# Kernel optimization log

Hardware: AMD Instinct MI355X
Metric: run time of the kernel (lower is better)

The kernel has to match this reference:

```python
import jax, jax.numpy as jnp
import numpy as np

B, T, H, K, V, O = 4, 2048, 512, 128, 128, 512


def setup_inputs() -> dict:
    key = jax.random.key(0)
    k0, k1, k2 = jax.random.split(key, 3)
    hidden_state = jax.random.normal(k0, (B, T, H), dtype=jnp.float32)
    cell_state = jnp.zeros((B, K, V), dtype=jnp.float32)
    # fused projection: hidden -> [query K, key K, gate K, value V]
    lim_p = np.sqrt(6.0 / (H + 3 * K + V)).astype(np.float32)  # xavier uniform
    proj_w = jax.random.uniform(k1, (3 * K + V, H), jnp.float32, -lim_p, lim_p)
    proj_b = jnp.zeros((3 * K + V,), jnp.float32)
    lim_o = np.sqrt(6.0 / (2 * V + O)).astype(np.float32)
    out_w = jax.random.uniform(k2, (O, 2 * V), jnp.float32, -lim_o, lim_o)
    out_b = jnp.zeros((O,), jnp.float32)
    return {"hidden_state": hidden_state, "cell_state": cell_state,
            "proj_w": proj_w, "proj_b": proj_b, "out_w": out_w, "out_b": out_b}


def reference(hidden_state, cell_state, proj_w, proj_b, out_w, out_b):
    Bq, Tq, _ = hidden_state.shape
    qkgv = hidden_state @ proj_w.T + proj_b          # (B,T,3K+V)
    query = qkgv[..., :K]
    kgate = jax.nn.sigmoid(qkgv[..., K:2 * K])       # key (sigmoid)
    gate = jax.nn.sigmoid(qkgv[..., 2 * K:3 * K])
    value = jnp.tanh(qkgv[..., 3 * K:])              # (B,T,V)

    def step(C, xs):
        q_t, k_t, g_t, v_t = xs                      # (B,K),(B,K),(B,K),(B,V)
        C = C * g_t[..., None] + k_t[..., None] * v_t[..., None, :]  # (B,K,V)
        o_t = jnp.einsum('bkv,bk->bv', C, q_t)       # C^T q
        return C, o_t

    xs = (query.swapaxes(0, 1), kgate.swapaxes(0, 1),
          gate.swapaxes(0, 1), value.swapaxes(0, 1))
    C_final, ov = jax.lax.scan(step, cell_state, xs)
    ov = ov.swapaxes(0, 1)                           # (B,T,V) output_val per step

    # causal Luong dot attention over the growing bank of past output_vals
    scores = jnp.einsum('btv,bsv->bts', ov, ov)      # (B,T,T)
    causal = jnp.tril(jnp.ones((Tq, Tq), dtype=bool))
    scores = jnp.where(causal, scores, -jnp.inf)
    attn = jax.nn.softmax(scores, axis=-1)
    context = jnp.einsum('bts,bsv->btv', attn, ov)   # (B,T,V)

    outputs = jnp.concatenate([ov, context], axis=-1) @ out_w.T + out_b  # (B,T,O)
    return outputs, C_final
```

## Files before the change

kernel.cpp:

```cpp
#include <hip/hip_runtime.h>
#include <hip/hip_bf16.h>


typedef __attribute__((ext_vector_type(8))) short bf16x8;
typedef __attribute__((ext_vector_type(4))) float f32x4;
typedef __attribute__((ext_vector_type(4))) short short4v;

#define MFMA(a,b,c) __builtin_amdgcn_mfma_f32_16x16x32_bf16(a,b,c,0,0,0)

__device__ __forceinline__ short f2b(float x){
  union { float f; unsigned u; } v; v.f = x;
  unsigned r = v.u + 0x7fffu + ((v.u >> 16) & 1u);
  return (short)(r >> 16);
}
__device__ __forceinline__ float b2f(short h){
  union { unsigned u; float f; } v;
  v.u = ((unsigned)(unsigned short)h) << 16;
  return v.f;
}
__device__ __forceinline__ void split2(float x, short& h, short& l){
  h = f2b(x);
  l = f2b(x - b2f(h));
}

__global__ void k_split(const float* __restrict__ in, short* __restrict__ hi,
                        short* __restrict__ lo, int n){
  int i = (blockIdx.x * blockDim.x + threadIdx.x) * 4;
  if (i < n){
    float4 v = *(const float4*)(in + i);
    short4v h, l;
    short th, tl;
    split2(v.x, th, tl); h.x = th; l.x = tl;
    split2(v.y, th, tl); h.y = th; l.y = tl;
    split2(v.z, th, tl); h.z = th; l.z = tl;
    split2(v.w, th, tl); h.w = th; l.w = tl;
    *(short4v*)(hi + i) = h;
    *(short4v*)(lo + i) = l;
  }
}

__global__ void k_cvt(const float* __restrict__ in, short* __restrict__ out, int n){
  int i = (blockIdx.x * blockDim.x + threadIdx.x) * 4;
  if (i < n){
    float4 v = *(const float4*)(in + i);
    short4v o; o.x = f2b(v.x); o.y = f2b(v.y); o.z = f2b(v.z); o.w = f2b(v.w);
    *(short4v*)(out + i) = o;
  }
}

__global__ __launch_bounds__(256) void k_gemm1(
    const short* __restrict__ Ah, const short* __restrict__ Al,
    const short* __restrict__ Bh, const short* __restrict__ Bl,
    const float* __restrict__ bias,
    float* __restrict__ q_o, float* __restrict__ kg_o,
    float* __restrict__ lg_o, float* __restrict__ vv_o)
{
  const int Kd = 512;
  __shared__ __align__(16) short Ash[128][40], Asl[128][40];
  __shared__ __align__(16) short Bsh[64][40],  Bsl[64][40];
  const int m0 = blockIdx.x * 128, n0 = blockIdx.y * 64;
  const int tid = threadIdx.x, lane = tid & 63, w = tid >> 6;
  const int wr = w >> 1, wc = w & 1;
  const int coll = lane & 15, rq = lane >> 4;
  f32x4 acc[4][2];
#pragma unroll
  for (int i = 0; i < 4; i++)
#pragma unroll
    for (int j = 0; j < 2; j++) acc[i][j] = (f32x4){0.f,0.f,0.f,0.f};

  const int ar = tid >> 1, ac = (tid & 1) * 16;
  const int br = tid >> 2, bc = (tid & 3) * 8;

  for (int k0 = 0; k0 < Kd; k0 += 32){
    __syncthreads();
    { size_t g = (size_t)(m0 + ar) * Kd + k0 + ac;
      *(bf16x8*)&Ash[ar][ac]     = *(const bf16x8*)(Ah + g);
      *(bf16x8*)&Ash[ar][ac + 8] = *(const bf16x8*)(Ah + g + 8);
      *(bf16x8*)&Asl[ar][ac]     = *(const bf16x8*)(Al + g);
      *(bf16x8*)&Asl[ar][ac + 8] = *(const bf16x8*)(Al + g + 8); }
    { size_t g = (size_t)(n0 + br) * Kd + k0 + bc;
      *(bf16x8*)&Bsh[br][bc] = *(const bf16x8*)(Bh + g);
      *(bf16x8*)&Bsl[br][bc] = *(const bf16x8*)(Bl + g); }
    __syncthreads();
    bf16x8 ah[4], al[4], bh[2], bl[2];
#pragma unroll
    for (int mi = 0; mi < 4; mi++){
      ah[mi] = *(const bf16x8*)&Ash[wr*64 + mi*16 + coll][rq*8];
      al[mi] = *(const bf16x8*)&Asl[wr*64 + mi*16 + coll][rq*8];
    }
#pragma unroll
    for (int ni = 0; ni < 2; ni++){
      bh[ni] = *(const bf16x8*)&Bsh[wc*32 + ni*16 + coll][rq*8];
      bl[ni] = *(const bf16x8*)&Bsl[wc*32 + ni*16 + coll][rq*8];
    }
#pragma unroll
    for (int mi = 0; mi < 4; mi++)
#pragma unroll
      for (int ni = 0; ni < 2; ni++){
        acc[mi][ni] = MFMA(ah[mi], bh[ni], acc[mi][ni]);
        acc[mi][ni] = MFMA(ah[mi], bl[ni], acc[mi][ni]);
        acc[mi][ni] = MFMA(al[mi], bh[ni], acc[mi][ni]);
      }
  }
#pragma unroll
  for (int mi = 0; mi < 4; mi++)
#pragma unroll
  for (int ni = 0; ni < 2; ni++){
    int gn = n0 + wc*32 + ni*16 + coll;
    float bsv = bias[gn];
    int sec = gn >> 7, jj = gn & 127;
#pragma unroll
    for (int r = 0; r < 4; r++){
      int gm = m0 + wr*64 + mi*16 + rq*4 + r;
      float v = acc[mi][ni][r] + bsv;
      size_t idx = (size_t)gm * 128 + jj;
      if (sec == 0)      q_o[idx] = v;
      else if (sec == 1) kg_o[idx] = 1.f / (1.f + __expf(-v));
      else if (sec == 2) lg_o[idx] = (v > 0.f) ? -log1pf(__expf(-v)) : (v - log1pf(__expf(v)));
      else               vv_o[idx] = tanhf(v);
    }
  }
}

__global__ __launch_bounds__(128) void k_prep(
  const float* __restrict__ q_f, const float* __restrict__ kg_f,
  const float* __restrict__ lg_f, const float* __restrict__ vv_f,
  short* __restrict__ qth, short* __restrict__ qtl,
  short* __restrict__ kth, short* __restrict__ ktl,
  short* __restrict__ khTh, short* __restrict__ khTl,
  short* __restrict__ vvTh, short* __restrict__ vvTl,
  float* __restrict__ Dend)
{
  const int bc = blockIdx.x;
  const int kx = threadIdx.x;
  const size_t base = ((size_t)(bc >> 6) * 2048 + (size_t)(bc & 63) * 32) * 128 + kx;
  double L[32];
  double Lr = 0.0;
#pragma unroll
  for (int s = 0; s < 32; s++){
    size_t idx = base + (size_t)s * 128;
    Lr += (double)lg_f[idx];
    L[s] = Lr;
    float lam  = __expf((float)Lr);
    float ilam = __expf((float)(-Lr));
    short h, l;
    split2(q_f[idx] * lam, h, l);  qth[idx] = h; qtl[idx] = l;
    split2(kg_f[idx] * ilam, h, l); kth[idx] = h; ktl[idx] = l;
  }
  const double Lend = Lr;
  Dend[(size_t)bc * 128 + kx] = (float)exp(Lend);
  __align__(16) short bufh[32], bufl[32];
#pragma unroll
  for (int s = 0; s < 32; s++){
    size_t idx = base + (size_t)s * 128;
    short h, l;
    split2(kg_f[idx] * __expf((float)(Lend - L[s])), h, l);
    bufh[s] = h; bufl[s] = l;
  }
  { short* dh = khTh + ((size_t)bc * 128 + kx) * 32;
    short* dl = khTl + ((size_t)bc * 128 + kx) * 32;
#pragma unroll
    for (int i = 0; i < 32; i += 8){
      *(bf16x8*)(dh + i) = *(const bf16x8*)(bufh + i);
      *(bf16x8*)(dl + i) = *(const bf16x8*)(bufl + i);
    } }
#pragma unroll
  for (int s = 0; s < 32; s++){
    short h, l;
    split2(vv_f[base + (size_t)s * 128], h, l);
    bufh[s] = h; bufl[s] = l;
  }
  { short* dh = vvTh + ((size_t)bc * 128 + kx) * 32;
    short* dl = vvTl + ((size_t)bc * 128 + kx) * 32;
#pragma unroll
    for (int i = 0; i < 32; i += 8){
      *(bf16x8*)(dh + i) = *(const bf16x8*)(bufh + i);
      *(bf16x8*)(dl + i) = *(const bf16x8*)(bufl + i);
    } }
}

__global__ __launch_bounds__(64) void k_scan(
  const short* __restrict__ khTh, const short* __restrict__ khTl,
  const short* __restrict__ vvTh, const short* __restrict__ vvTl,
  const float* __restrict__ Dend, const float* __restrict__ cell0,
  short* __restrict__ sth, short* __restrict__ stl, float* __restrict__ Cfin)
{
  const int blk = blockIdx.x;
  const int b = blk >> 6, tile = blk & 63;
  const int kt = tile >> 3, vt = tile & 7;
  const int lane = threadIdx.x & 63;
  const int coll = lane & 15, rq = lane >> 4;
  const int kcol = kt*16 + coll;
  const int vrow0 = vt*16 + rq*4;
  const size_t cb0 = (size_t)b * 64;

  f32x4 acc;
#pragma unroll
  for (int r = 0; r < 4; r++)
    acc[r] = cell0[((size_t)b*128 + kcol)*128 + vrow0 + r];

  size_t gv = (cb0*128 + vt*16 + coll)*32 + rq*8;
  size_t gk = (cb0*128 + kt*16 + coll)*32 + rq*8;
  bf16x8 avh = *(const bf16x8*)(vvTh + gv);
  bf16x8 avl = *(const bf16x8*)(vvTl + gv);
  bf16x8 bkh = *(const bf16x8*)(khTh + gk);
  bf16x8 bkl = *(const bf16x8*)(khTl + gk);
  float d = Dend[cb0*128 + kcol];

  for (int ck = 0; ck < 64; ck++){
    const size_t cb = cb0 + ck;
    const size_t cbn = cb0 + (ck < 63 ? ck + 1 : ck);
    size_t ngv = (cbn*128 + vt*16 + coll)*32 + rq*8;
    size_t ngk = (cbn*128 + kt*16 + coll)*32 + rq*8;
    bf16x8 navh = *(const bf16x8*)(vvTh + ngv);
    bf16x8 navl = *(const bf16x8*)(vvTl + ngv);
    bf16x8 nbkh = *(const bf16x8*)(khTh + ngk);
    bf16x8 nbkl = *(const bf16x8*)(khTl + ngk);
    float nd = Dend[cbn*128 + kcol];
    {
      size_t sb = (cb*128 + vrow0)*128 + kcol;
#pragma unroll
      for (int r = 0; r < 4; r++){
        short h, l; split2(acc[r], h, l);
        sth[sb + (size_t)r*128] = h;
        stl[sb + (size_t)r*128] = l;
      }
    }
#pragma unroll
    for (int r = 0; r < 4; r++) acc[r] *= d;
    acc = MFMA(avh, bkh, acc);
    acc = MFMA(avh, bkl, acc);
    acc = MFMA(avl, bkh, acc);
    avh = navh; avl = navl; bkh = nbkh; bkl = nbkl; d = nd;
  }
  *(f32x4*)(Cfin + ((size_t)b*128 + kcol)*128 + vrow0) = acc;
}

__global__ __launch_bounds__(256) void k_chunkout(
  const short* __restrict__ qth, const short* __restrict__ qtl,
  const short* __restrict__ kth, const short* __restrict__ ktl,
  const short* __restrict__ vvTh, const short* __restrict__ vvTl,
  const short* __restrict__ sth, const short* __restrict__ stl,
  short* __restrict__ ovT, short* __restrict__ ovc,
  short* __restrict__ ovqh, short* __restrict__ ovql)
{
  __shared__ __align__(16) short ATh[32][40], ATl[32][40];
  const int bc = blockIdx.x;
  const int b = bc >> 6, ck = bc & 63;
  const int tid = threadIdx.x, lane = tid & 63, w = tid >> 6;
  const int coll = lane & 15, rq = lane >> 4;
  const size_t tbase = (size_t)b * 2048 + (size_t)ck * 32;
  {
    const int si = w >> 1, ti = w & 1;
    f32x4 aA = (f32x4){0.f,0.f,0.f,0.f};
#pragma unroll
    for (int kit = 0; kit < 4; kit++){
      size_t ga = (tbase + si*16 + coll) * 128 + kit*32 + rq*8;
      size_t gb = (tbase + ti*16 + coll) * 128 + kit*32 + rq*8;
      bf16x8 a3h = *(const bf16x8*)(kth + ga), a3l = *(const bf16x8*)(ktl + ga);
      bf16x8 b3h = *(const bf16x8*)(qth + gb), b3l = *(const bf16x8*)(qtl + gb);
      aA = MFMA(a3h, b3h, aA);
      aA = MFMA(a3h, b3l, aA);
      aA = MFMA(a3l, b3h, aA);
    }
#pragma unroll
    for (int r = 0; r < 4; r++){
      int s = si*16 + rq*4 + r, t = ti*16 + coll;
      float val = (s <= t) ? aA[r] : 0.f;
      short h, l; split2(val, h, l);
      ATh[t][s] = h; ATl[t][s] = l;
    }
  }
  __syncthreads();
  const int vb = w * 32;
  f32x4 o[2][2];
#pragma unroll
  for (int vi = 0; vi < 2; vi++)
#pragma unroll
    for (int ti = 0; ti < 2; ti++) o[vi][ti] = (f32x4){0.f,0.f,0.f,0.f};
#pragma unroll
  for (int kit = 0; kit < 4; kit++){
    bf16x8 aCh[2], aCl[2], bqh[2], bql[2];
#pragma unroll
    for (int vi = 0; vi < 2; vi++){
      size_t g = ((size_t)bc * 128 + vb + vi*16 + coll) * 128 + kit*32 + rq*8;
      aCh[vi] = *(const bf16x8*)(sth + g);
      aCl[vi] = *(const bf16x8*)(stl + g);
    }
#pragma unroll
    for (int ti = 0; ti < 2; ti++){
      size_t g = (tbase + ti*16 + coll) * 128 + kit*32 + rq*8;
      bqh[ti] = *(const bf16x8*)(qth + g);
      bql[ti] = *(const bf16x8*)(qtl + g);
    }
#pragma unroll
    for (int vi = 0; vi < 2; vi++)
#pragma unroll
      for (int ti = 0; ti < 2; ti++){
        o[vi][ti] = MFMA(aCh[vi], bqh[ti], o[vi][ti]);
        o[vi][ti] = MFMA(aCh[vi], bql[ti], o[vi][ti]);
        o[vi][ti] = MFMA(aCl[vi], bqh[ti], o[vi][ti]);
      }
  }
  {
    bf16x8 a2h[2], a2l[2], b2h[2], b2l[2];
#pragma unroll
    for (int vi = 0; vi < 2; vi++){
      size_t g = ((size_t)bc * 128 + vb + vi*16 + coll) * 32 + rq*8;
      a2h[vi] = *(const bf16x8*)(vvTh + g);
      a2l[vi] = *(const bf16x8*)(vvTl + g);
    }
#pragma unroll
    for (int ti = 0; ti < 2; ti++){
      b2h[ti] = *(const bf16x8*)&ATh[ti*16 + coll][rq*8];
      b2l[ti] = *(const bf16x8*)&ATl[ti*16 + coll][rq*8];
    }
#pragma unroll
    for (int vi = 0; vi < 2; vi++)
#pragma unroll
      for (int ti = 0; ti < 2; ti++){
        o[vi][ti] = MFMA(a2h[vi], b2h[ti], o[vi][ti]);
        o[vi][ti] = MFMA(a2h[vi], b2l[ti], o[vi][ti]);
        o[vi][ti] = MFMA(a2l[vi], b2h[ti], o[vi][ti]);
      }
  }
#pragma unroll
  for (int vi = 0; vi < 2; vi++)
#pragma unroll
  for (int ti = 0; ti < 2; ti++)
#pragma unroll
  for (int r = 0; r < 4; r++){
    int v = vb + vi*16 + rq*4 + r;
    int tl = ti*16 + coll;
    float val = o[vi][ti][r];
    short h, l; split2(val, h, l);
    ovT[((size_t)b * 128 + v) * 2048 + (size_t)ck * 32 + tl] = h;
    ovc[(tbase + tl) * 256 + v] = h;
    ovqh[(tbase + tl) * 128 + v] = h;
    ovql[(tbase + tl) * 128 + v] = l;
  }
}

__global__ __launch_bounds__(256) void k_attn(
  const short* __restrict__ ovqh, const short* __restrict__ ovql,
  const short* __restrict__ ovT,
  float* __restrict__ m_part, float* __restrict__ l_part,
  short* __restrict__ oa_part)
{
  const int qi = blockIdx.x, b = blockIdx.y, p = blockIdx.z;
  const int qbase = qi * 64;
  const int ps = p * 256;
  const size_t obase = (size_t)b * 2048;
  const int tid = threadIdx.x;
  if (ps > qbase + 63){
    if (tid < 64) l_part[((obase + qbase + tid) << 3) + p] = 0.f;
    return;
  }
  __shared__ __align__(16) short P[4][16][40];
  const int lane = tid & 63, w = tid >> 6;
  const int coll = lane & 15, rq = lane >> 4;
  const int tw = qbase + w * 16;
  bf16x8 qfh[4], qfl[4];
#pragma unroll
  for (int kit = 0; kit < 4; kit++){
    size_t g = (obase + tw + coll) * 128 + kit*32 + rq*8;
    qfh[kit] = *(const bf16x8*)(ovqh + g);
    qfl[kit] = *(const bf16x8*)(ovql + g);
  }
  float m[4], l[4];
  f32x4 oa[8];
#pragma unroll
  for (int r = 0; r < 4; r++){ m[r] = -1e30f; l[r] = 0.f; }
#pragma unroll
  for (int df = 0; df < 8; df++) oa[df] = (f32x4){0.f,0.f,0.f,0.f};
  const int send = min(tw + 15, ps + 255);
  for (int s0 = ps; s0 <= send; s0 += 32){
    f32x4 sc[2];
#pragma unroll
    for (int sf = 0; sf < 2; sf++){
      bf16x8 kh[4], kl[4];
#pragma unroll
      for (int kit = 0; kit < 4; kit++){
        size_t g = (obase + s0 + sf*16 + coll) * 128 + kit*32 + rq*8;
        kh[kit] = *(const bf16x8*)(ovqh + g);
        kl[kit] = *(const bf16x8*)(ovql + g);
      }
      f32x4 c0 = (f32x4){0.f,0.f,0.f,0.f};
      f32x4 c1 = (f32x4){0.f,0.f,0.f,0.f};
      f32x4 c2 = (f32x4){0.f,0.f,0.f,0.f};
#pragma unroll
      for (int kit = 0; kit < 4; kit++){
        c0 = MFMA(qfh[kit], kh[kit], c0);
        c1 = MFMA(qfh[kit], kl[kit], c1);
        c2 = MFMA(qfl[kit], kh[kit], c2);
      }
      sc[sf] = c0 + c1 + c2;
    }
    bf16x8 vf[8];
#pragma unroll
    for (int df = 0; df < 8; df++)
      vf[df] = *(const bf16x8*)(ovT + ((size_t)b*128 + df*16 + coll)*2048 + s0 + rq*8);
#pragma unroll
    for (int r = 0; r < 4; r++){
      int trow = tw + rq*4 + r;
      float s0v = (s0 + coll      <= trow) ? sc[0][r] : -1e30f;
      float s1v = (s0 + 16 + coll <= trow) ? sc[1][r] : -1e30f;
      float mx = fmaxf(s0v, s1v);
#pragma unroll
      for (int d = 1; d < 16; d <<= 1) mx = fmaxf(mx, __shfl_xor(mx, d));
      float mn = fmaxf(m[r], mx);
      float scale = __expf(m[r] - mn);
      float p0 = __expf(s0v - mn);
      float p1 = __expf(s1v - mn);
      float rs = p0 + p1;
#pragma unroll
      for (int d = 1; d < 16; d <<= 1) rs += __shfl_xor(rs, d);
      l[r] = l[r] * scale + rs;
      m[r] = mn;
#pragma unroll
      for (int df = 0; df < 8; df++) oa[df][r] *= scale;
      P[w][rq*4 + r][coll]      = f2b(p0);
      P[w][rq*4 + r][16 + coll] = f2b(p1);
    }
    bf16x8 pf = *(const bf16x8*)&P[w][coll][rq*8];
#pragma unroll
    for (int df = 0; df < 8; df++)
      oa[df] = MFMA(pf, vf[df], oa[df]);
  }
#pragma unroll
  for (int r = 0; r < 4; r++){
    int t = tw + rq*4 + r;
    size_t idx8 = ((obase + t) << 3) + p;
    if (coll == 0){ m_part[idx8] = m[r]; l_part[idx8] = l[r]; }
#pragma unroll
    for (int df = 0; df < 8; df++)
      oa_part[idx8*128 + df*16 + coll] = f2b(oa[df][r]);
  }
}

__global__ __launch_bounds__(256) void k_comb(
  const float* __restrict__ m_part, const float* __restrict__ l_part,
  const short* __restrict__ oa_part, short* __restrict__ ovc)
{
  const int blk = blockIdx.x;
  const int b = blk >> 5, qi = blk & 31;
  const int row = threadIdx.x >> 2, cg = threadIdx.x & 3;
  const int t = qi*64 + row;
  const size_t base8 = ((size_t)b*2048 + t) * 8;
  float mv[8], lv[8];
#pragma unroll
  for (int p = 0; p < 8; p++){ mv[p] = m_part[base8+p]; lv[p] = l_part[base8+p]; }
  float M = -3e38f;
#pragma unroll
  for (int p = 0; p < 8; p++) if (lv[p] > 0.f) M = fmaxf(M, mv[p]);
  float L = 0.f, wgt[8];
#pragma unroll
  for (int p = 0; p < 8; p++){
    wgt[p] = (lv[p] > 0.f) ? __expf(mv[p] - M) : 0.f;
    L += lv[p] * wgt[p];
  }
  const float inv = 1.f / L;
  const int v0 = cg * 32;
  float acc[32];
#pragma unroll
  for (int j = 0; j < 32; j++) acc[j] = 0.f;
#pragma unroll
  for (int p = 0; p < 8; p++){
    if (lv[p] > 0.f){
      const short* src = oa_part + (base8 + p)*128 + v0;
#pragma unroll
      for (int jo = 0; jo < 32; jo += 8){
        bf16x8 x = *(const bf16x8*)(src + jo);
#pragma unroll
        for (int j = 0; j < 8; j++) acc[jo+j] += b2f(x[j]) * wgt[p];
      }
    }
  }
  short* dst = ovc + ((size_t)b*2048 + t)*256 + 128 + v0;
#pragma unroll
  for (int jo = 0; jo < 32; jo += 8){
    bf16x8 o;
#pragma unroll
    for (int j = 0; j < 8; j++) o[j] = f2b(acc[jo+j] * inv);
    *(bf16x8*)(dst + jo) = o;
  }
}

__global__ __launch_bounds__(256) void k_gemm0(
  const short* __restrict__ A, const short* __restrict__ Bw,
  const float* __restrict__ bias, float* __restrict__ out)
{
  const int Kd = 256, N = 512;
  __shared__ __align__(16) short As[128][40];
  __shared__ __align__(16) short Bs[64][40];
  const int m0 = blockIdx.x * 128, n0 = blockIdx.y * 64;
  const int tid = threadIdx.x, lane = tid & 63, w = tid >> 6;
  const int wr = w >> 1, wc = w & 1;
  const int coll = lane & 15, rq = lane >> 4;
  f32x4 acc[4][2];
#pragma unroll
  for (int i = 0; i < 4; i++)
#pragma unroll
    for (int j = 0; j < 2; j++) acc[i][j] = (f32x4){0.f,0.f,0.f,0.f};
  const int ar = tid >> 1, ac = (tid & 1) * 16;
  const int br = tid >> 2, bc = (tid & 3) * 8;
  for (int k0 = 0; k0 < Kd; k0 += 32){
    __syncthreads();
    { const short* g = A + (size_t)(m0 + ar) * Kd + k0 + ac;
      *(bf16x8*)&As[ar][ac]     = *(const bf16x8*)g;
      *(bf16x8*)&As[ar][ac + 8] = *(const bf16x8*)(g + 8); }
    { const short* g = Bw + (size_t)(n0 + br) * Kd + k0 + bc;
      *(bf16x8*)&Bs[br][bc] = *(const bf16x8*)g; }
    __syncthreads();
    bf16x8 a[4], b[2];
#pragma unroll
    for (int mi = 0; mi < 4; mi++) a[mi] = *(const bf16x8*)&As[wr*64 + mi*16 + coll][rq*8];
#pragma unroll
    for (int ni = 0; ni < 2; ni++) b[ni] = *(const bf16x8*)&Bs[wc*32 + ni*16 + coll][rq*8];
#pragma unroll
    for (int mi = 0; mi < 4; mi++)
#pragma unroll
      for (int ni = 0; ni < 2; ni++) acc[mi][ni] = MFMA(a[mi], b[ni], acc[mi][ni]);
  }
#pragma unroll
  for (int mi = 0; mi < 4; mi++)
#pragma unroll
  for (int ni = 0; ni < 2; ni++){
    int gn = n0 + wc*32 + ni*16 + coll;
    float bsv = bias[gn];
#pragma unroll
    for (int r = 0; r < 4; r++){
      int gm = m0 + wr*64 + mi*16 + rq*4 + r;
      out[(size_t)gm * N + gn] = acc[mi][ni][r] + bsv;
    }
  }
}

extern "C" void kernel_launch(void* const* d_in, const int* in_sizes, int n_in,
                              void* d_out, int out_size, void* d_ws, size_t ws_size,
                              hipStream_t stream){
  const float* hidden = (const float*)d_in[0];
  const float* cell0  = (const float*)d_in[1];
  const float* projw  = (const float*)d_in[2];
  const float* projb  = (const float*)d_in[3];
  const float* outw   = (const float*)d_in[4];
  const float* outb   = (const float*)d_in[5];
  float* out = (float*)d_out;

  char* ws = (char*)d_ws;
  size_t off = 0;
  auto alloc = [&](size_t bytes) -> void* {
    void* p = ws + off;
    off += (bytes + 255) & ~(size_t)255;
    return p;
  };
  short* Xh   = (short*)alloc(8192ULL * 512 * 2);
  short* Xl   = (short*)alloc(8192ULL * 512 * 2);
  short* ovqh = Xh;
  short* ovql = Xh + 1048576;
  short* ovT  = Xh + 2097152;
  short* ovc  = Xh + 3145728;
  float* q_f  = (float*)alloc(8192ULL * 128 * 4);
  float* kg_f = (float*)alloc(8192ULL * 128 * 4);
  float* lg_f = (float*)alloc(8192ULL * 128 * 4);
  float* vv_f = (float*)alloc(8192ULL * 128 * 4);
  short* sth  = (short*)q_f;
  short* stl  = sth + 4194304;
  short* oa_part = (short*)q_f;
  short* Wh   = (short*)alloc(512ULL * 512 * 2);
  short* Wl   = (short*)alloc(512ULL * 512 * 2);
  short* OWbf = (short*)alloc(512ULL * 256 * 2);
  short* qth  = (short*)alloc(8192ULL * 128 * 2);
  short* qtl  = (short*)alloc(8192ULL * 128 * 2);
  short* kth  = (short*)alloc(8192ULL * 128 * 2);
  short* ktl  = (short*)alloc(8192ULL * 128 * 2);
  short* khTh = (short*)alloc(256ULL * 128 * 32 * 2);
  short* khTl = (short*)alloc(256ULL * 128 * 32 * 2);
  short* vvTh = (short*)alloc(256ULL * 128 * 32 * 2);
  short* vvTl = (short*)alloc(256ULL * 128 * 32 * 2);
  float* Dend = (float*)alloc(256ULL * 128 * 4);
  float* m_part = (float*)alloc(4ULL * 2048 * 8 * 4);
  float* l_part = (float*)alloc(4ULL * 2048 * 8 * 4);

  k_split<<<4096, 256, 0, stream>>>(hidden, Xh, Xl, 8192 * 512);
  k_split<<<256,  256, 0, stream>>>(projw,  Wh, Wl, 512 * 512);
  k_cvt<<<128, 256, 0, stream>>>(outw, OWbf, 512 * 256);

  k_gemm1<<<dim3(64, 8), 256, 0, stream>>>(Xh, Xl, Wh, Wl, projb, q_f, kg_f, lg_f, vv_f);
  k_prep<<<256, 128, 0, stream>>>(q_f, kg_f, lg_f, vv_f,
                                  qth, qtl, kth, ktl, khTh, khTl, vvTh, vvTl, Dend);
  k_scan<<<256, 64, 0, stream>>>(khTh, khTl, vvTh, vvTl, Dend, cell0,
                                 sth, stl, out + 8192ULL * 512);
  k_chunkout<<<256, 256, 0, stream>>>(qth, qtl, kth, ktl, vvTh, vvTl, sth, stl,
                                      ovT, ovc, ovqh, ovql);
  k_attn<<<dim3(32, 4, 8), 256, 0, stream>>>(ovqh, ovql, ovT, m_part, l_part, oa_part);
  k_comb<<<128, 256, 0, stream>>>(m_part, l_part, oa_part, ovc);
  k_gemm0<<<dim3(64, 8), 256, 0, stream>>>(ovc, OWbf, outb, out);
}
```

Baseline: 293.8 us.

## Use direct global-to-LDS loads with XOR-swizzled tiles in projection and output GEMMs

Both bf16 GEMM kernels now stage tiles with global_load_lds 16-byte direct copies into unpadded 64-wide LDS tiles, using an XOR swizzle to avoid bank conflicts instead of row padding. The K-step grows from 32 to 64, which halves the barrier count. The split-precision GEMM is restructured into three sequential passes over K (hi*hi, hi*lo, lo*hi) instead of three MFMAs per loaded tile. This removes the register round-trip for global loads but adds more total A/B traffic in gemm1, since each operand is reloaded per pass, and there is still no double buffering.

New measurement: 293.8 us. Within noise of the previous version (-0.0%).

```diff
diff --git a/kernel.cpp b/kernel.cpp
--- a/kernel.cpp
+++ b/kernel.cpp
@@ -21,6 +21,11 @@
 __device__ __forceinline__ void split2(float x, short& h, short& l){
   h = f2b(x);
   l = f2b(x - b2f(h));
+}
+__device__ __forceinline__ void gload16(const void* g, void* l){
+  __builtin_amdgcn_global_load_lds(
+    (__attribute__((address_space(1))) unsigned int*)(void*)(g),
+    (__attribute__((address_space(3))) unsigned int*)(l), 16, 0, 0);
 }
 
 __global__ void k_split(const float* __restrict__ in, short* __restrict__ hi,
@@ -55,10 +60,10 @@
     float* __restrict__ q_o, float* __restrict__ kg_o,
     float* __restrict__ lg_o, float* __restrict__ vv_o)
 {
-  const int Kd = 512;
-  __shared__ __align__(16) short Ash[128][40], Asl[128][40];
-  __shared__ __align__(16) short Bsh[64][40],  Bsl[64][40];
-  const int m0 = blockIdx.x * 128, n0 = blockIdx.y * 64;
+  __shared__ __align__(16) short At[128*64];
+  __shared__ __align__(16) short Bt[64*64];
+  const int m0 = blockIdx.x * 128;
+  const int ny = blockIdx.y;
   const int tid = threadIdx.x, lane = tid & 63, w = tid >> 6;
   const int wr = w >> 1, wc = w & 1;
   const int coll = lane & 15, rq = lane >> 4;
@@ -68,47 +73,56 @@
 #pragma unroll
     for (int j = 0; j < 2; j++) acc[i][j] = (f32x4){0.f,0.f,0.f,0.f};
 
-  const int ar = tid >> 1, ac = (tid & 1) * 16;
-  const int br = tid >> 2, bc = (tid & 3) * 8;
-
-  for (int k0 = 0; k0 < Kd; k0 += 32){
+  for (int step = 0; step < 24; ++step){
+    const int seg = step >> 3;
+    const int k0 = (step & 7) * 64;
+    const short* Asrc = (seg < 2) ? Ah : Al;
+    const short* Bsrc = (seg == 1) ? Bl : Bh;
     __syncthreads();
-    { size_t g = (size_t)(m0 + ar) * Kd + k0 + ac;
-      *(bf16x8*)&Ash[ar][ac]     = *(const bf16x8*)(Ah + g);
-      *(bf16x8*)&Ash[ar][ac + 8] = *(const bf16x8*)(Ah + g + 8);
-      *(bf16x8*)&Asl[ar][ac]     = *(const bf16x8*)(Al + g);
-      *(bf16x8*)&Asl[ar][ac + 8] = *(const bf16x8*)(Al + g + 8); }
-    { size_t g = (size_t)(n0 + br) * Kd + k0 + bc;
-      *(bf16x8*)&Bsh[br][bc] = *(const bf16x8*)(Bh + g);
-      *(bf16x8*)&Bsl[br][bc] = *(const bf16x8*)(Bl + g); }
+#pragma unroll
+    for (int t = 0; t < 4; ++t){
+      int ci = t*256 + tid;
+      int row = ci >> 3;
+      int cs = (ci & 7) ^ (row & 7);
+      gload16(Asrc + (size_t)(m0 + row)*512 + k0 + cs*8, At + ci*8);
+    }
+#pragma unroll
+    for (int t = 0; t < 2; ++t){
+      int ci = t*256 + tid;
+      int row = ci >> 3;
+      int cs = (ci & 7) ^ (row & 7);
+      gload16(Bsrc + (size_t)(ny*64 + row)*512 + k0 + cs*8, Bt + ci*8);
+    }
     __syncthreads();
-    bf16x8 ah[4], al[4], bh[2], bl[2];
-#pragma unroll
-    for (int mi = 0; mi < 4; mi++){
-      ah[mi] = *(const bf16x8*)&Ash[wr*64 + mi*16 + coll][rq*8];
-      al[mi] = *(const bf16x8*)&Asl[wr*64 + mi*16 + coll][rq*8];
-    }
-#pragma unroll
-    for (int ni = 0; ni < 2; ni++){
-      bh[ni] = *(const bf16x8*)&Bsh[wc*32 + ni*16 + coll][rq*8];
-      bl[ni] = *(const bf16x8*)&Bsl[wc*32 + ni*16 + coll][rq*8];
-    }
-#pragma unroll
-    for (int mi = 0; mi < 4; mi++)
+#pragma unroll
+    for (int kk = 0; kk < 2; ++kk){
+      bf16x8 a[4], b[2];
+#pragma unroll
+      for (int mi = 0; mi < 4; mi++){
+        int ar = wr*64 + mi*16 + coll;
+        a[mi] = *(const bf16x8*)&At[ar*64 + (((kk*4+rq) ^ (ar & 7))*8)];
+      }
 #pragma unroll
       for (int ni = 0; ni < 2; ni++){
-        acc[mi][ni] = MFMA(ah[mi], bh[ni], acc[mi][ni]);
-        acc[mi][ni] = MFMA(ah[mi], bl[ni], acc[mi][ni]);
-        acc[mi][ni] = MFMA(al[mi], bh[ni], acc[mi][ni]);
-      }
-  }
+        int br = wc*32 + ni*16 + coll;
+        b[ni] = *(const bf16x8*)&Bt[br*64 + (((kk*4+rq) ^ (br & 7))*8)];
+      }
+#pragma unroll
+      for (int mi = 0; mi < 4; mi++)
+#pragma unroll
+        for (int ni = 0; ni < 2; ni++)
+          acc[mi][ni] = MFMA(a[mi], b[ni], acc[mi][ni]);
+    }
+  }
+  const int sec = ny >> 1;
+  const int jb  = (ny & 1) * 64;
 #pragma unroll
   for (int mi = 0; mi < 4; mi++)
 #pragma unroll
   for (int ni = 0; ni < 2; ni++){
-    int gn = n0 + wc*32 + ni*16 + coll;
-    float bsv = bias[gn];
-    int sec = gn >> 7, jj = gn & 127;
+    int gl = wc*32 + ni*16 + coll;
+    float bsv = bias[ny*64 + gl];
+    int jj = jb + gl;
 #pragma unroll
     for (int r = 0; r < 4; r++){
       int gm = m0 + wr*64 + mi*16 + rq*4 + r;
@@ -490,10 +504,10 @@
   const short* __restrict__ A, const short* __restrict__ Bw,
   const float* __restrict__ bias, float* __restrict__ out)
 {
-  const int Kd = 256, N = 512;
-  __shared__ __align__(16) short As[128][40];
-  __shared__ __align__(16) short Bs[64][40];
-  const int m0 = blockIdx.x * 128, n0 = blockIdx.y * 64;
+  __shared__ __align__(16) short At[128*64];
+  __shared__ __align__(16) short Bt[64*64];
+  const int m0 = blockIdx.x * 128;
+  const int ny = blockIdx.y;
   const int tid = threadIdx.x, lane = tid & 63, w = tid >> 6;
   const int wr = w >> 1, wc = w & 1;
   const int coll = lane & 15, rq = lane >> 4;
@@ -502,36 +516,55 @@
   for (int i = 0; i < 4; i++)
 #pragma unroll
     for (int j = 0; j < 2; j++) acc[i][j] = (f32x4){0.f,0.f,0.f,0.f};
-  const int ar = tid >> 1, ac = (tid & 1) * 16;
-  const int br = tid >> 2, bc = (tid & 3) * 8;
-  for (int k0 = 0; k0 < Kd; k0 += 32){
+
+  for (int step = 0; step < 4; ++step){
+    const int k0 = step * 64;
     __syncthreads();
-    { const short* g = A + (size_t)(m0 + ar) * Kd + k0 + ac;
-      *(bf16x8*)&As[ar][ac]     = *(const bf16x8*)g;
-      *(bf16x8*)&As[ar][ac + 8] = *(const bf16x8*)(g + 8); }
-    { const short* g = Bw + (size_t)(n0 + br) * Kd + k0 + bc;
-      *(bf16x8*)&Bs[br][bc] = *(const bf16x8*)g; }
+#pragma unroll
+    for (int t = 0; t < 4; ++t){
+      int ci = t*256 + tid;
+      int row = ci >> 3;
+      int cs = (ci & 7) ^ (row & 7);
+      gload16(A + (size_t)(m0 + row)*256 + k0 + cs*8, At + ci*8);
+    }
+#pragma unroll
+    for (int t = 0; t < 2; ++t){
+      int ci = t*256 + tid;
+      int row = ci >> 3;
+      int cs = (ci & 7) ^ (row & 7);
+      gload16(Bw + (size_t)(ny*64 + row)*256 + k0 + cs*8, Bt + ci*8);
+    }
     __syncthreads();
-    bf16x8 a[4], b[2];
-#pragma unroll
-    for (int mi = 0; mi < 4; mi++) a[mi] = *(const bf16x8*)&As[wr*64 + mi*16 + coll][rq*8];
-#pragma unroll
-    for (int ni = 0; ni < 2; ni++) b[ni] = *(const bf16x8*)&Bs[wc*32 + ni*16 + coll][rq*8];
-#pragma unroll
-    for (int mi = 0; mi < 4; mi++)
-#pragma unroll
-      for (int ni = 0; ni < 2; ni++) acc[mi][ni] = MFMA(a[mi], b[ni], acc[mi][ni]);
+#pragma unroll
+    for (int kk = 0; kk < 2; ++kk){
+      bf16x8 a[4], b[2];
+#pragma unroll
+      for (int mi = 0; mi < 4; mi++){
+        int ar = wr*64 + mi*16 + coll;
+        a[mi] = *(const bf16x8*)&At[ar*64 + (((kk*4+rq) ^ (ar & 7))*8)];
+      }
+#pragma unroll
+      for (int ni = 0; ni < 2; ni++){
+        int br = wc*32 + ni*16 + coll;
+        b[ni] = *(const bf16x8*)&Bt[br*64 + (((kk*4+rq) ^ (br & 7))*8)];
+      }
+#pragma unroll
+      for (int mi = 0; mi < 4; mi++)
+#pragma unroll
+        for (int ni = 0; ni < 2; ni++)
+          acc[mi][ni] = MFMA(a[mi], b[ni], acc[mi][ni]);
+    }
   }
 #pragma unroll
   for (int mi = 0; mi < 4; mi++)
 #pragma unroll
   for (int ni = 0; ni < 2; ni++){
-    int gn = n0 + wc*32 + ni*16 + coll;
+    int gn = ny*64 + wc*32 + ni*16 + coll;
     float bsv = bias[gn];
 #pragma unroll
     for (int r = 0; r < 4; r++){
       int gm = m0 + wr*64 + mi*16 + rq*4 + r;
-      out[(size_t)gm * N + gn] = acc[mi][ni][r] + bsv;
+      out[(size_t)gm * 512 + gn] = acc[mi][ni][r] + bsv;
     }
   }
 }
```

## Drop LDS staging in projection GEMMs, load MFMA fragments straight from global

Applied to the files above, without the earlier changes.

Both GEMM kernels (the input projection with split-bf16 and the output projection) stop staging tiles in shared memory with barriers. Instead each wave loads its MFMA operand fragments directly from global memory and computes a 64x64 tile, with a block covering 64 rows by 256 columns. This removes the __syncthreads and LDS round trips. In exchange it depends on L1/L2 to absorb repeated A-row loads across the four waves, and it issues less coalesced 16-byte-per-lane global reads.

After: 395.7 us. 34.7% more time.

```diff
diff --git a/kernel.cpp b/kernel.cpp
--- a/kernel.cpp
+++ b/kernel.cpp
@@ -55,63 +55,51 @@
     float* __restrict__ q_o, float* __restrict__ kg_o,
     float* __restrict__ lg_o, float* __restrict__ vv_o)
 {
-  const int Kd = 512;
-  __shared__ __align__(16) short Ash[128][40], Asl[128][40];
-  __shared__ __align__(16) short Bsh[64][40],  Bsl[64][40];
-  const int m0 = blockIdx.x * 128, n0 = blockIdx.y * 64;
   const int tid = threadIdx.x, lane = tid & 63, w = tid >> 6;
-  const int wr = w >> 1, wc = w & 1;
   const int coll = lane & 15, rq = lane >> 4;
-  f32x4 acc[4][2];
+  const int m0 = blockIdx.x * 64;
+  const int n0 = blockIdx.y * 256 + w * 64;
+  f32x4 acc[4][4];
 #pragma unroll
   for (int i = 0; i < 4; i++)
 #pragma unroll
-    for (int j = 0; j < 2; j++) acc[i][j] = (f32x4){0.f,0.f,0.f,0.f};
-
-  const int ar = tid >> 1, ac = (tid & 1) * 16;
-  const int br = tid >> 2, bc = (tid & 3) * 8;
-
-  for (int k0 = 0; k0 < Kd; k0 += 32){
-    __syncthreads();
-    { size_t g = (size_t)(m0 + ar) * Kd + k0 + ac;
-      *(bf16x8*)&Ash[ar][ac]     = *(const bf16x8*)(Ah + g);
-      *(bf16x8*)&Ash[ar][ac + 8] = *(const bf16x8*)(Ah + g + 8);
-      *(bf16x8*)&Asl[ar][ac]     = *(const bf16x8*)(Al + g);
-      *(bf16x8*)&Asl[ar][ac + 8] = *(const bf16x8*)(Al + g + 8); }
-    { size_t g = (size_t)(n0 + br) * Kd + k0 + bc;
-      *(bf16x8*)&Bsh[br][bc] = *(const bf16x8*)(Bh + g);
-      *(bf16x8*)&Bsl[br][bc] = *(const bf16x8*)(Bl + g); }
-    __syncthreads();
-    bf16x8 ah[4], al[4], bh[2], bl[2];
+    for (int j = 0; j < 4; j++) acc[i][j] = (f32x4){0.f,0.f,0.f,0.f};
+
+#pragma unroll 2
+  for (int k0 = 0; k0 < 512; k0 += 32){
+    bf16x8 ah[4], al[4], bh[4], bl[4];
 #pragma unroll
     for (int mi = 0; mi < 4; mi++){
-      ah[mi] = *(const bf16x8*)&Ash[wr*64 + mi*16 + coll][rq*8];
-      al[mi] = *(const bf16x8*)&Asl[wr*64 + mi*16 + coll][rq*8];
-    }
-#pragma unroll
-    for (int ni = 0; ni < 2; ni++){
-      bh[ni] = *(const bf16x8*)&Bsh[wc*32 + ni*16 + coll][rq*8];
-      bl[ni] = *(const bf16x8*)&Bsl[wc*32 + ni*16 + coll][rq*8];
+      size_t g = (size_t)(m0 + mi*16 + coll)*512 + k0 + rq*8;
+      ah[mi] = *(const bf16x8*)(Ah + g);
+      al[mi] = *(const bf16x8*)(Al + g);
+    }
+#pragma unroll
+    for (int ni = 0; ni < 4; ni++){
+      size_t g = (size_t)(n0 + ni*16 + coll)*512 + k0 + rq*8;
+      bh[ni] = *(const bf16x8*)(Bh + g);
+      bl[ni] = *(const bf16x8*)(Bl + g);
     }
 #pragma unroll
     for (int mi = 0; mi < 4; mi++)
 #pragma unroll
-      for (int ni = 0; ni < 2; ni++){
+      for (int ni = 0; ni < 4; ni++){
         acc[mi][ni] = MFMA(ah[mi], bh[ni], acc[mi][ni]);
         acc[mi][ni] = MFMA(ah[mi], bl[ni], acc[mi][ni]);
         acc[mi][ni] = MFMA(al[mi], bh[ni], acc[mi][ni]);
       }
   }
+  const int sec = n0 >> 7;
 #pragma unroll
   for (int mi = 0; mi < 4; mi++)
 #pragma unroll
-  for (int ni = 0; ni < 2; ni++){
-    int gn = n0 + wc*32 + ni*16 + coll;
-    float bsv = bias[gn];
-    int sec = gn >> 7, jj = gn & 127;
+  for (int ni = 0; ni < 4; ni++){
+    int gcol = n0 + ni*16 + coll;
+    float bsv = bias[gcol];
+    int jj = gcol & 127;
 #pragma unroll
     for (int r = 0; r < 4; r++){
-      int gm = m0 + wr*64 + mi*16 + rq*4 + r;
+      int gm = m0 + mi*16 + rq*4 + r;
       float v = acc[mi][ni][r] + bsv;
       size_t idx = (size_t)gm * 128 + jj;
       if (sec == 0)      q_o[idx] = v;
@@ -490,48 +478,45 @@
   const short* __restrict__ A, const short* __restrict__ Bw,
   const float* __restrict__ bias, float* __restrict__ out)
 {
-  const int Kd = 256, N = 512;
-  __shared__ __align__(16) short As[128][40];
-  __shared__ __align__(16) short Bs[64][40];
-  const int m0 = blockIdx.x * 128, n0 = blockIdx.y * 64;
   const int tid = threadIdx.x, lane = tid & 63, w = tid >> 6;
-  const int wr = w >> 1, wc = w & 1;
   const int coll = lane & 15, rq = lane >> 4;
-  f32x4 acc[4][2];
+  const int m0 = blockIdx.x * 64;
+  const int n0 = blockIdx.y * 256 + w * 64;
+  f32x4 acc[4][4];
 #pragma unroll
   for (int i = 0; i < 4; i++)
 #pragma unroll
-    for (int j = 0; j < 2; j++) acc[i][j] = (f32x4){0.f,0.f,0.f,0.f};
-  const int ar = tid >> 1, ac = (tid & 1) * 16;
-  const int br = tid >> 2, bc = (tid & 3) * 8;
-  for (int k0 = 0; k0 < Kd; k0 += 32){
-    __syncthreads();
-    { const short* g = A + (size_t)(m0 + ar) * Kd + k0 + ac;
-      *(bf16x8*)&As[ar][ac]     = *(const bf16x8*)g;
-      *(bf16x8*)&As[ar][ac + 8] = *(const bf16x8*)(g + 8); }
-    { const short* g = Bw + (size_t)(n0 + br) * Kd + k0 + bc;
-      *(bf16x8*)&Bs[br][bc] = *(const bf16x8*)g; }
-    __syncthreads();
-    bf16x8 a[4], b[2];
-#pragma unroll
-    for (int mi = 0; mi < 4; mi++) a[mi] = *(const bf16x8*)&As[wr*64 + mi*16 + coll][rq*8];
-#pragma unroll
-    for (int ni = 0; ni < 2; ni++) b[ni] = *(const bf16x8*)&Bs[wc*32 + ni*16 + coll][rq*8];
+    for (int j = 0; j < 4; j++) acc[i][j] = (f32x4){0.f,0.f,0.f,0.f};
+
+#pragma unroll 2
+  for (int k0 = 0; k0 < 256; k0 += 32){
+    bf16x8 a[4], b[4];
+#pragma unroll
+    for (int mi = 0; mi < 4; mi++){
+      size_t g = (size_t)(m0 + mi*16 + coll)*256 + k0 + rq*8;
+      a[mi] = *(const bf16x8*)(A + g);
+    }
+#pragma unroll
+    for (int ni = 0; ni < 4; ni++){
+      size_t g = (size_t)(n0 + ni*16 + coll)*256 + k0 + rq*8;
+      b[ni] = *(const bf16x8*)(Bw + g);
+    }
 #pragma unroll
     for (int mi = 0; mi < 4; mi++)
 #pragma unroll
-      for (int ni = 0; ni < 2; ni++) acc[mi][ni] = MFMA(a[mi], b[ni], acc[mi][ni]);
+      for (int ni = 0; ni < 4; ni++)
+        acc[mi][ni] = MFMA(a[mi], b[ni], acc[mi][ni]);
   }
 #pragma unroll
   for (int mi = 0; mi < 4; mi++)
 #pragma unroll
-  for (int ni = 0; ni < 2; ni++){
-    int gn = n0 + wc*32 + ni*16 + coll;
-    float bsv = bias[gn];
+  for (int ni = 0; ni < 4; ni++){
+    int gcol = n0 + ni*16 + coll;
+    float bsv = bias[gcol];
 #pragma unroll
     for (int r = 0; r < 4; r++){
-      int gm = m0 + wr*64 + mi*16 + rq*4 + r;
-      out[(size_t)gm * N + gn] = acc[mi][ni][r] + bsv;
+      int gm = m0 + mi*16 + rq*4 + r;
+      out[(size_t)gm * 512 + gcol] = acc[mi][ni][r] + bsv;
     }
   }
 }
@@ -586,7 +571,7 @@
   k_split<<<256,  256, 0, stream>>>(projw,  Wh, Wl, 512 * 512);
   k_cvt<<<128, 256, 0, stream>>>(outw, OWbf, 512 * 256);
 
-  k_gemm1<<<dim3(64, 8), 256, 0, stream>>>(Xh, Xl, Wh, Wl, projb, q_f, kg_f, lg_f, vv_f);
+  k_gemm1<<<dim3(128, 2), 256, 0, stream>>>(Xh, Xl, Wh, Wl, projb, q_f, kg_f, lg_f, vv_f);
   k_prep<<<256, 128, 0, stream>>>(q_f, kg_f, lg_f, vv_f,
                                   qth, qtl, kth, ktl, khTh, khTl, vvTh, vvTl, Dend);
   k_scan<<<256, 64, 0, stream>>>(khTh, khTl, vvTh, vvTl, Dend, cell0,
@@ -595,5 +580,5 @@
                                       ovT, ovc, ovqh, ovql);
   k_attn<<<dim3(32, 4, 8), 256, 0, stream>>>(ovqh, ovql, ovT, m_part, l_part, oa_part);
   k_comb<<<128, 256, 0, stream>>>(m_part, l_part, oa_part, ovc);
-  k_gemm0<<<dim3(64, 8), 256, 0, stream>>>(ovc, OWbf, outb, out);
-}
+  k_gemm0<<<dim3(128, 2), 256, 0, stream>>>(ovc, OWbf, outb, out);
+}
```
